# Optimization experiments

Measured on AMD Instinct MI355X. Metric: run time of the kernel, lower is better.

## Reference

```python
import jax, jax.numpy as jnp
import numpy as np

E = 2048
H = 16
D = E // H  # head_dim = 128


def setup_inputs() -> dict:
    key = jax.random.key(0)
    ks = jax.random.split(key, 8)
    s = 0.02
    x = jax.random.normal(ks[0], (2, 2048, E), dtype=jnp.float32)
    Wq = jax.random.normal(ks[1], (E, E), dtype=jnp.float32) * s
    Wk = jax.random.normal(ks[2], (E, E), dtype=jnp.float32) * s
    Wv = jax.random.normal(ks[3], (E, E), dtype=jnp.float32) * s
    W1 = jax.random.normal(ks[4], (2 * E, E), dtype=jnp.float32) * s
    b1 = jax.random.normal(ks[5], (2 * E,), dtype=jnp.float32) * s
    W2 = jax.random.normal(ks[6], (E, 2 * E), dtype=jnp.float32) * s
    b2 = jax.random.normal(ks[7], (E,), dtype=jnp.float32) * s
    return {"x": x, "Wq": Wq, "Wk": Wk, "Wv": Wv, "W1": W1, "b1": b1, "W2": W2, "b2": b2}


def reference(x, Wq, Wk, Wv, W1, b1, W2, b2):
    B, S, _ = x.shape
    # QKV projections (torch Linear: x @ W.T), reshape to (B,S,H,D)
    q = (x @ Wq.T).reshape(B, S, H, D)
    k = (x @ Wk.T).reshape(B, S, H, D)
    v = (x @ Wv.T).reshape(B, S, H, D)
    # scores: (B,H,S,S)
    score = jnp.einsum('bqhd,bkhd->bhqk', q, k)
    # causal mask added BEFORE scaling (as in original; -inf unaffected by scale)
    causal = jnp.tril(jnp.ones((S, S), dtype=bool))
    score = jnp.where(causal, score, -jnp.inf)
    score = score / jnp.sqrt(jnp.float32(D))
    attn = jax.nn.softmax(score, axis=-1)
    o = jnp.einsum('bhqk,bkhd->bqhd', attn, v).reshape(B, S, E)
    # FFN with hidden = 2*E, no residual connections in this block
    h = jax.nn.gelu(o @ W1.T + b1)
    return h @ W2.T + b2
```

## Files before the change

kernel.cpp:

```cpp
#include <hip/hip_runtime.h>
#include <cmath>


typedef _Float16 half8 __attribute__((ext_vector_type(8)));
typedef _Float16 half4v __attribute__((ext_vector_type(4)));
typedef float float4v __attribute__((ext_vector_type(4)));

__device__ inline void load_lds16(const _Float16* g, _Float16* l) {
  __builtin_amdgcn_global_load_lds(
      (const __attribute__((address_space(1))) void*)g,
      (__attribute__((address_space(3))) void*)l, 16, 0, 0);
}

__global__ void cvt_kernel(const float* __restrict__ s0, const float* __restrict__ s1,
                           const float* __restrict__ s2, const float* __restrict__ s3,
                           _Float16* d0, _Float16* d1, _Float16* d2, _Float16* d3,
                           int n0, int n1, int n2, int n3, float sc1) {
  const float* s;
  _Float16* d;
  int n;
  float sc = 1.0f;
  switch (blockIdx.y) {
    case 0: s = s0; d = d0; n = n0; break;
    case 1: s = s1; d = d1; n = n1; sc = sc1; break;
    case 2: s = s2; d = d2; n = n2; break;
    default: s = s3; d = d3; n = n3; break;
  }
  const int step = gridDim.x * 256 * 4;
  for (int i = (blockIdx.x * 256 + threadIdx.x) * 4; i < n; i += step) {
    float4v v = *(const float4v*)&s[i];
    half4v h;
#pragma unroll
    for (int e = 0; e < 4; e++) h[e] = (_Float16)(v[e] * sc);
    *(half4v*)&d[i] = h;
  }
}

__device__ inline void gemm_core(const _Float16* __restrict__ A,
                                 const _Float16* __restrict__ B, int K, int bm,
                                 int bn, _Float16* As, _Float16* Bs,
                                 float4v acc[4][4]) {
  const int tid = threadIdx.x;
  const int wave = tid >> 6, lane = tid & 63;
  const int l16 = lane & 15, quad = lane >> 4;
  const int wm = (wave & 1) * 64, wn = (wave >> 1) * 64;
  const int r0 = tid >> 2, c0 = (tid & 3) * 8;
  const int lds0 = (wave * 64) * 8;
  const int lds1 = (256 + wave * 64) * 8;

  for (int k0 = 0; k0 < K; k0 += 32) {
    load_lds16(&A[(size_t)(bm + r0) * K + k0 + c0], &As[lds0]);
    load_lds16(&A[(size_t)(bm + 64 + r0) * K + k0 + c0], &As[lds1]);
    load_lds16(&B[(size_t)(bn + r0) * K + k0 + c0], &Bs[lds0]);
    load_lds16(&B[(size_t)(bn + 64 + r0) * K + k0 + c0], &Bs[lds1]);
    __syncthreads();

    half8 af[4], bf[4];
#pragma unroll
    for (int i = 0; i < 4; i++)
      af[i] = *(const half8*)&As[(wm + i * 16 + l16) * 32 + quad * 8];
#pragma unroll
    for (int j = 0; j < 4; j++)
      bf[j] = *(const half8*)&Bs[(wn + j * 16 + l16) * 32 + quad * 8];

#pragma unroll
    for (int i = 0; i < 4; i++)
#pragma unroll
      for (int j = 0; j < 4; j++)
        acc[i][j] = __builtin_amdgcn_mfma_f32_16x16x32_f16(af[i], bf[j], acc[i][j], 0, 0, 0);
    __syncthreads();
  }
}

__global__ __launch_bounds__(256, 3) void gemm_qkv(
    const _Float16* __restrict__ xh, const _Float16* __restrict__ Wq,
    const _Float16* __restrict__ Wk, const _Float16* __restrict__ Wv,
    _Float16* __restrict__ Qh, _Float16* __restrict__ Kh,
    _Float16* __restrict__ Vt) {
  __shared__ __align__(16) _Float16 As[4096];
  __shared__ __align__(16) _Float16 Bs[4096];
  const int z = blockIdx.z;
  const _Float16* B = (z == 0) ? Wq : (z == 1 ? Wk : Wv);
  const int bm = blockIdx.y * 128, bn = blockIdx.x * 128;
  float4v acc[4][4] = {};
  gemm_core(xh, B, 2048, bm, bn, As, Bs, acc);

  const int tid = threadIdx.x;
  const int wave = tid >> 6, lane = tid & 63;
  const int l16 = lane & 15, quad = lane >> 4;
  const int wm = (wave & 1) * 64, wn = (wave >> 1) * 64;
  _Float16* outRM = z ? Kh : Qh;
#pragma unroll
  for (int j = 0; j < 4; j++) {
    const int col = bn + wn + j * 16 + l16;
#pragma unroll
    for (int i = 0; i < 4; i++) {
      const int rbase = bm + wm + i * 16 + quad * 4;
#pragma unroll
      for (int reg = 0; reg < 4; reg++) {
        const int m = rbase + reg;
        const _Float16 hv = (_Float16)acc[i][j][reg];
        if (z == 2)
          Vt[((size_t)(m >> 11) << 22) + ((size_t)col << 11) + (m & 2047)] = hv;
        else
          outRM[(size_t)m * 2048 + col] = hv;
      }
    }
  }
}

template <bool GELU>
__global__ __launch_bounds__(256, 3) void gemm_ffn(
    const _Float16* __restrict__ A, const _Float16* __restrict__ B,
    const float* __restrict__ bias, void* __restrict__ out, int M, int N,
    int K) {
  __shared__ __align__(16) _Float16 As[4096];
  __shared__ __align__(16) _Float16 Bs[4096];
  const int bm = blockIdx.y * 128, bn = blockIdx.x * 128;
  float4v acc[4][4] = {};
  gemm_core(A, B, K, bm, bn, As, Bs, acc);

  const int tid = threadIdx.x;
  const int wave = tid >> 6, lane = tid & 63;
  const int l16 = lane & 15, quad = lane >> 4;
  const int wm = (wave & 1) * 64, wn = (wave >> 1) * 64;
#pragma unroll
  for (int j = 0; j < 4; j++) {
    const int col = bn + wn + j * 16 + l16;
    const float bv = bias[col];
#pragma unroll
    for (int i = 0; i < 4; i++) {
      const int rbase = bm + wm + i * 16 + quad * 4;
#pragma unroll
      for (int reg = 0; reg < 4; reg++) {
        const int m = rbase + reg;
        float v = acc[i][j][reg] + bv;
        if (GELU) {
          const float x = v;
          const float inner = 0.7978845608028654f * (x + 0.044715f * x * x * x);
          v = 0.5f * x * (1.0f + tanhf(inner));
          ((_Float16*)out)[(size_t)m * N + col] = (_Float16)v;
        } else {
          ((float*)out)[(size_t)m * N + col] = v;
        }
      }
    }
  }
}

__global__ __launch_bounds__(256, 2) void attn_mfma(
    const _Float16* __restrict__ Qh, const _Float16* __restrict__ Kh,
    const _Float16* __restrict__ Vt, _Float16* __restrict__ Oh) {
  __shared__ __align__(16) _Float16 Ksh[64][136];
  __shared__ __align__(16) _Float16 Vsh[128][72];
  __shared__ __align__(16) _Float16 Psh[4][32][72];

  const int b = blockIdx.z;
  int qt = blockIdx.x;
  if (b) qt = gridDim.x - 1 - qt;
  const int h = blockIdx.y;
  const int tid = threadIdx.x;
  const int wave = tid >> 6, lane = tid & 63;
  const int l16 = lane & 15, quad = lane >> 4;
  const int q0 = qt * 128;
  const int wq0 = q0 + wave * 32;

  half8 qf[2][4];
#pragma unroll
  for (int rb = 0; rb < 2; rb++)
#pragma unroll
    for (int kc = 0; kc < 4; kc++)
      qf[rb][kc] = *(const half8*)(Qh +
          (size_t)(b * 2048 + wq0 + rb * 16 + l16) * 2048 + h * 128 +
          kc * 32 + quad * 8);

  half8 ones;
#pragma unroll
  for (int e = 0; e < 8; e++) ones[e] = (_Float16)1.0f;

  const int kkey = tid >> 2, kd = (tid & 3) * 32;
  const int vd = tid >> 1, vkey = (tid & 1) * 32;

  half8 kpre[4], vpre[4];
  {
    const _Float16* p = Kh + (size_t)(b * 2048 + kkey) * 2048 + h * 128 + kd;
#pragma unroll
    for (int i = 0; i < 4; i++) kpre[i] = *(const half8*)(p + i * 8);
    const _Float16* pv = Vt + ((size_t)b << 22) + (size_t)(h * 128 + vd) * 2048 + vkey;
#pragma unroll
    for (int i = 0; i < 4; i++) vpre[i] = *(const half8*)(pv + i * 8);
  }

  float4v o[2][9] = {};
  float4v mrow[2];
#pragma unroll
  for (int rb = 0; rb < 2; rb++)
#pragma unroll
    for (int e = 0; e < 4; e++) mrow[rb][e] = -INFINITY;

  const int nkb = qt * 2 + 2;
  for (int kb = 0; kb < nkb; kb++) {
    const int k0 = kb * 64;
    __syncthreads();
#pragma unroll
    for (int i = 0; i < 4; i++) *(half8*)&Ksh[kkey][kd + i * 8] = kpre[i];
#pragma unroll
    for (int i = 0; i < 4; i++) *(half8*)&Vsh[vd][vkey + i * 8] = vpre[i];
    __syncthreads();

    if (kb + 1 < nkb) {
      const int k1 = k0 + 64;
      const _Float16* p = Kh + (size_t)(b * 2048 + k1 + kkey) * 2048 + h * 128 + kd;
#pragma unroll
      for (int i = 0; i < 4; i++) kpre[i] = *(const half8*)(p + i * 8);
      const _Float16* pv = Vt + ((size_t)b << 22) + (size_t)(h * 128 + vd) * 2048 + k1 + vkey;
#pragma unroll
      for (int i = 0; i < 4; i++) vpre[i] = *(const half8*)(pv + i * 8);
    }

    if (k0 <= wq0 + 31) {
      float4v s[2][4] = {};
#pragma unroll
      for (int kc = 0; kc < 4; kc++) {
#pragma unroll
        for (int cb = 0; cb < 4; cb++) {
          half8 kf = *(const half8*)&Ksh[cb * 16 + l16][kc * 32 + quad * 8];
#pragma unroll
          for (int rb = 0; rb < 2; rb++)
            s[rb][cb] = __builtin_amdgcn_mfma_f32_16x16x32_f16(qf[rb][kc], kf, s[rb][cb], 0, 0, 0);
        }
      }
      if (k0 + 63 > wq0) {
#pragma unroll
        for (int cb = 0; cb < 4; cb++)
#pragma unroll
          for (int rb = 0; rb < 2; rb++)
#pragma unroll
            for (int reg = 0; reg < 4; reg++) {
              const int key = k0 + cb * 16 + l16;
              const int row = wq0 + rb * 16 + quad * 4 + reg;
              if (key > row) s[rb][cb][reg] = -INFINITY;
            }
      }
#pragma unroll
      for (int rb = 0; rb < 2; rb++) {
        float4v mt;
#pragma unroll
        for (int e = 0; e < 4; e++)
          mt[e] = fmaxf(fmaxf(s[rb][0][e], s[rb][1][e]),
                        fmaxf(s[rb][2][e], s[rb][3][e]));
#pragma unroll
        for (int msk = 1; msk <= 8; msk <<= 1)
#pragma unroll
          for (int e = 0; e < 4; e++) mt[e] = fmaxf(mt[e], __shfl_xor(mt[e], msk, 64));
        int need = 0;
#pragma unroll
        for (int e = 0; e < 4; e++) need |= (mt[e] > mrow[rb][e] + 8.0f) ? 1 : 0;
        if (__any(need)) {
          float4v al;
#pragma unroll
          for (int e = 0; e < 4; e++) {
            const float mn = fmaxf(mrow[rb][e], mt[e]);
            al[e] = exp2f(mrow[rb][e] - mn);
            mrow[rb][e] = mn;
          }
#pragma unroll
          for (int cd = 0; cd < 9; cd++)
#pragma unroll
            for (int e = 0; e < 4; e++) o[rb][cd][e] *= al[e];
        }
#pragma unroll
        for (int cb = 0; cb < 4; cb++) {
#pragma unroll
          for (int e = 0; e < 4; e++) s[rb][cb][e] = exp2f(s[rb][cb][e] - mrow[rb][e]);
#pragma unroll
          for (int e = 0; e < 4; e++)
            Psh[wave][rb * 16 + quad * 4 + e][cb * 16 + l16] = (_Float16)s[rb][cb][e];
        }
      }
      half8 pf[2][2];
#pragma unroll
      for (int rb = 0; rb < 2; rb++)
#pragma unroll
        for (int kc = 0; kc < 2; kc++)
          pf[rb][kc] = *(const half8*)&Psh[wave][rb * 16 + l16][kc * 32 + quad * 8];
#pragma unroll
      for (int cd = 0; cd < 8; cd++) {
#pragma unroll
        for (int kc = 0; kc < 2; kc++) {
          half8 vf = *(const half8*)&Vsh[cd * 16 + l16][kc * 32 + quad * 8];
#pragma unroll
          for (int rb = 0; rb < 2; rb++)
            o[rb][cd] = __builtin_amdgcn_mfma_f32_16x16x32_f16(pf[rb][kc], vf, o[rb][cd], 0, 0, 0);
        }
      }
#pragma unroll
      for (int kc = 0; kc < 2; kc++)
#pragma unroll
        for (int rb = 0; rb < 2; rb++)
          o[rb][8] = __builtin_amdgcn_mfma_f32_16x16x32_f16(pf[rb][kc], ones, o[rb][8], 0, 0, 0);
    }
  }

#pragma unroll
  for (int rb = 0; rb < 2; rb++) {
    float4v inv;
#pragma unroll
    for (int e = 0; e < 4; e++) inv[e] = 1.0f / o[rb][8][e];
#pragma unroll
    for (int cd = 0; cd < 8; cd++)
#pragma unroll
      for (int reg = 0; reg < 4; reg++)
        Oh[(size_t)(b * 2048 + wq0 + rb * 16 + quad * 4 + reg) * 2048 +
           h * 128 + cd * 16 + l16] = (_Float16)(o[rb][cd][reg] * inv[reg]);
  }
}

extern "C" void kernel_launch(void* const* d_in, const int* in_sizes, int n_in,
                              void* d_out, int out_size, void* d_ws,
                              size_t ws_size, hipStream_t stream) {
  const float* x = (const float*)d_in[0];
  const float* Wq = (const float*)d_in[1];
  const float* Wk = (const float*)d_in[2];
  const float* Wv = (const float*)d_in[3];
  const float* W1 = (const float*)d_in[4];
  const float* b1 = (const float*)d_in[5];
  const float* W2 = (const float*)d_in[6];
  const float* b2 = (const float*)d_in[7];
  float* out = (float*)d_out;

  const int ME = 8388608;
  const int EE = 4194304;

  _Float16* ws = (_Float16*)d_ws;
  _Float16* xh  = ws;
  _Float16* Wqh = xh + ME;
  _Float16* Wkh = Wqh + EE;
  _Float16* Wvh = Wkh + EE;
  _Float16* Qh  = Wvh + EE;
  _Float16* Kh  = Qh + ME;
  _Float16* Vt  = Kh + ME;
  _Float16* Oh  = xh;
  _Float16* W1h = Wqh;
  _Float16* W2h = Vt;
  _Float16* Hid = Qh;

  const float qscale = 1.4426950408889634f * 0.08838834764831845f;

  cvt_kernel<<<dim3(1024, 4), 256, 0, stream>>>(x, Wq, Wk, Wv, xh, Wqh, Wkh, Wvh,
                                                ME, EE, EE, EE, qscale);
  gemm_qkv<<<dim3(16, 32, 3), 256, 0, stream>>>(xh, Wqh, Wkh, Wvh, Qh, Kh, Vt);
  attn_mfma<<<dim3(16, 16, 2), 256, 0, stream>>>(Qh, Kh, Vt, Oh);
  cvt_kernel<<<dim3(1024, 2), 256, 0, stream>>>(W1, W2, nullptr, nullptr,
                                                W1h, W2h, nullptr, nullptr,
                                                ME, ME, 0, 0, 1.0f);
  gemm_ffn<true><<<dim3(32, 32), 256, 0, stream>>>(Oh, W1h, b1, Hid, 4096, 4096, 2048);
  gemm_ffn<false><<<dim3(16, 32), 256, 0, stream>>>(Hid, W2h, b2, out, 4096, 2048, 4096);
}
```

Before: 602.5 us.

## Replace GEMM core with 256x256 tiles, 8 waves and double-buffered LDS pipeline

Swaps the simple 128x128, 4-wave GEMM core for a 256x256 tile core run by 512 threads. It double-buffers 64-wide K slices in 128KB of LDS, interleaves async global-to-LDS loads with MFMA quarters under explicit barriers and waitcnts, and swizzles the LDS layout to avoid bank conflicts. The aim is more data reuse per tile and memory latency hidden behind MFMA work in all three projection/FFN GEMMs. The cost is fewer blocks (256 for the smaller GEMMs on 256 CUs) and high register and LDS pressure, and the hand-tuned barrier schedule is fragile to get right.

```diff
diff --git a/kernel.cpp b/kernel.cpp
--- a/kernel.cpp
+++ b/kernel.cpp
@@ -36,70 +36,147 @@
   }
 }
 
-__device__ inline void gemm_core(const _Float16* __restrict__ A,
-                                 const _Float16* __restrict__ B, int K, int bm,
-                                 int bn, _Float16* As, _Float16* Bs,
-                                 float4v acc[4][4]) {
+__device__ __forceinline__ void gemm8_core(
+    const _Float16* __restrict__ A, const _Float16* __restrict__ B, int K,
+    int bm, int bn, _Float16* lds, float4v acc[8][4]) {
   const int tid = threadIdx.x;
-  const int wave = tid >> 6, lane = tid & 63;
+  const int w = tid >> 6, lane = tid & 63;
   const int l16 = lane & 15, quad = lane >> 4;
-  const int wm = (wave & 1) * 64, wn = (wave >> 1) * 64;
-  const int r0 = tid >> 2, c0 = (tid & 3) * 8;
-  const int lds0 = (wave * 64) * 8;
-  const int lds1 = (256 + wave * 64) * 8;
-
-  for (int k0 = 0; k0 < K; k0 += 32) {
-    load_lds16(&A[(size_t)(bm + r0) * K + k0 + c0], &As[lds0]);
-    load_lds16(&A[(size_t)(bm + 64 + r0) * K + k0 + c0], &As[lds1]);
-    load_lds16(&B[(size_t)(bn + r0) * K + k0 + c0], &Bs[lds0]);
-    load_lds16(&B[(size_t)(bn + 64 + r0) * K + k0 + c0], &Bs[lds1]);
-    __syncthreads();
-
-    half8 af[4], bf[4];
-#pragma unroll
-    for (int i = 0; i < 4; i++)
-      af[i] = *(const half8*)&As[(wm + i * 16 + l16) * 32 + quad * 8];
-#pragma unroll
-    for (int j = 0; j < 4; j++)
-      bf[j] = *(const half8*)&Bs[(wn + j * 16 + l16) * 32 + quad * 8];
-
-#pragma unroll
-    for (int i = 0; i < 4; i++)
-#pragma unroll
-      for (int j = 0; j < 4; j++)
-        acc[i][j] = __builtin_amdgcn_mfma_f32_16x16x32_f16(af[i], bf[j], acc[i][j], 0, 0, 0);
-    __syncthreads();
-  }
-}
-
-__global__ __launch_bounds__(256, 3) void gemm_qkv(
+  const int srow = w * 16 + (lane >> 2);
+  const int clocal = ((lane & 3) * 8) ^ ((lane & 32) ? 16 : 0);
+  int rdh = (l16 << 5) + (quad << 3);
+  rdh ^= (l16 & 8) << 1;
+
+  const _Float16* pA0 = A + (size_t)(bm + srow) * K + clocal;
+  const _Float16* pA1 = A + (size_t)(bm + 128 + srow) * K + clocal;
+  const _Float16* pB0 = B + (size_t)(bn + srow) * K + clocal;
+  const _Float16* pB1 = B + (size_t)(bn + 128 + srow) * K + clocal;
+
+  _Float16* const dA0 = lds + w * 1024;
+  _Float16* const dA1 = lds + 8192 + w * 1024;
+  _Float16* const dB0 = lds + 16384 + w * 1024;
+  _Float16* const dB1 = lds + 24576 + w * 1024;
+
+  const int aH = w >> 2, bH = (w >> 1) & 1, bRB = (w & 1) * 4;
+  const _Float16* const rA0 = lds + aH * 8192;
+  const _Float16* const rB0 = lds + 16384 + bH * 8192;
+  const _Float16* const rA1 = rA0 + 32768;
+  const _Float16* const rB1 = rB0 + 32768;
+
+  const int NT = K >> 6;
+
+#define STG(p, d, kt)                     \
+  do {                                    \
+    const _Float16* _s = (p) + (kt) * 64; \
+    load_lds16(_s, (d));                  \
+    load_lds16(_s + 32, (d) + 512);       \
+  } while (0)
+#define BARRIER() asm volatile("s_barrier" ::: "memory")
+#define WAIT_LGKM()                                  \
+  asm volatile("s_waitcnt lgkmcnt(0)" ::: "memory"); \
+  __builtin_amdgcn_sched_barrier(0);
+#define RD_A(base, RB0)                                                       \
+  _Pragma("unroll") for (int rb = 0; rb < 4; rb++)                            \
+  _Pragma("unroll") for (int ks = 0; ks < 2; ks++)                            \
+      af[rb][ks] = *(const half8*)&(base)[((((RB0) + rb) * 2 + ks) << 9) + rdh];
+#define RD_B(base, J0)                                                        \
+  _Pragma("unroll") for (int j = 0; j < 2; j++)                               \
+  _Pragma("unroll") for (int ks = 0; ks < 2; ks++)                            \
+      bf[(J0) + j][ks] =                                                      \
+          *(const half8*)&(base)[(((bRB + (J0) + j) * 2 + ks) << 9) + rdh];
+#define MFMA_Q(RB0, J0)                                                       \
+  __builtin_amdgcn_s_setprio(1);                                              \
+  _Pragma("unroll") for (int rb = 0; rb < 4; rb++)                            \
+  _Pragma("unroll") for (int j = 0; j < 2; j++)                               \
+  _Pragma("unroll") for (int ks = 0; ks < 2; ks++)                            \
+      acc[(RB0) + rb][(J0) + j] = __builtin_amdgcn_mfma_f32_16x16x32_f16(     \
+          af[rb][ks], bf[(J0) + j][ks], acc[(RB0) + rb][(J0) + j], 0, 0, 0);  \
+  __builtin_amdgcn_s_setprio(0);                                              \
+  BARRIER();
+
+  STG(pB0, dB0, 0); STG(pB1, dB1, 0); STG(pA0, dA0, 0); STG(pA1, dA1, 0);
+  STG(pB0, dB0 + 32768, 1); STG(pB1, dB1 + 32768, 1);
+  asm volatile("s_waitcnt vmcnt(4)" ::: "memory");
+  BARRIER();
+
+  half8 af[4][2], bf[4][2];
+
+  for (int t = 0; t < NT; t += 2) {
+    const bool last = (t + 2 >= NT);
+    RD_A(rA0, 0) RD_B(rB0, 0)
+    STG(pA0, dA0 + 32768, t + 1);
+    BARRIER(); WAIT_LGKM()
+    MFMA_Q(0, 0)
+    RD_B(rB0, 2)
+    STG(pA1, dA1 + 32768, t + 1);
+    BARRIER(); WAIT_LGKM()
+    MFMA_Q(0, 2)
+    RD_A(rA0, 4)
+    if (!last) STG(pB0, dB0, t + 2);
+    BARRIER(); WAIT_LGKM()
+    MFMA_Q(4, 0)
+    if (!last) {
+      STG(pA0, dA0, t + 2);
+      asm volatile("s_waitcnt vmcnt(4)" ::: "memory");
+    } else {
+      asm volatile("s_waitcnt vmcnt(0)" ::: "memory");
+    }
+    BARRIER();
+    MFMA_Q(4, 2)
+    RD_A(rA1, 0) RD_B(rB1, 0)
+    if (!last) STG(pA1, dA1, t + 2);
+    BARRIER(); WAIT_LGKM()
+    MFMA_Q(0, 0)
+    RD_B(rB1, 2)
+    if (!last) STG(pB1, dB1, t + 2);
+    BARRIER(); WAIT_LGKM()
+    MFMA_Q(0, 2)
+    RD_A(rA1, 4)
+    if (!last) STG(pB0, dB0 + 32768, t + 3);
+    BARRIER(); WAIT_LGKM()
+    MFMA_Q(4, 0)
+    if (!last) {
+      STG(pB1, dB1 + 32768, t + 3);
+      asm volatile("s_waitcnt vmcnt(4)" ::: "memory");
+    }
+    BARRIER();
+    MFMA_Q(4, 2)
+  }
+#undef STG
+#undef BARRIER
+#undef WAIT_LGKM
+#undef RD_A
+#undef RD_B
+#undef MFMA_Q
+}
+
+__global__ __launch_bounds__(512, 2) void gemm_qkv(
     const _Float16* __restrict__ xh, const _Float16* __restrict__ Wq,
     const _Float16* __restrict__ Wk, const _Float16* __restrict__ Wv,
     _Float16* __restrict__ Qh, _Float16* __restrict__ Kh,
     _Float16* __restrict__ Vt) {
-  __shared__ __align__(16) _Float16 As[4096];
-  __shared__ __align__(16) _Float16 Bs[4096];
+  __shared__ __align__(16) _Float16 lds[65536];
   const int z = blockIdx.z;
   const _Float16* B = (z == 0) ? Wq : (z == 1 ? Wk : Wv);
-  const int bm = blockIdx.y * 128, bn = blockIdx.x * 128;
-  float4v acc[4][4] = {};
-  gemm_core(xh, B, 2048, bm, bn, As, Bs, acc);
+  const int bm = blockIdx.y * 256, bn = blockIdx.x * 256;
+  float4v acc[8][4] = {};
+  gemm8_core(xh, B, 2048, bm, bn, lds, acc);
 
   const int tid = threadIdx.x;
-  const int wave = tid >> 6, lane = tid & 63;
+  const int w = tid >> 6, lane = tid & 63;
   const int l16 = lane & 15, quad = lane >> 4;
-  const int wm = (wave & 1) * 64, wn = (wave >> 1) * 64;
+  const int wm = (w >> 2) * 128, wn = (w & 3) * 64;
   _Float16* outRM = z ? Kh : Qh;
 #pragma unroll
   for (int j = 0; j < 4; j++) {
     const int col = bn + wn + j * 16 + l16;
 #pragma unroll
-    for (int i = 0; i < 4; i++) {
-      const int rbase = bm + wm + i * 16 + quad * 4;
+    for (int rb = 0; rb < 8; rb++) {
+      const int rbase = bm + wm + rb * 16 + quad * 4;
 #pragma unroll
       for (int reg = 0; reg < 4; reg++) {
         const int m = rbase + reg;
-        const _Float16 hv = (_Float16)acc[i][j][reg];
+        const _Float16 hv = (_Float16)acc[rb][j][reg];
         if (z == 2)
           Vt[((size_t)(m >> 11) << 22) + ((size_t)col << 11) + (m & 2047)] = hv;
         else
@@ -110,31 +187,29 @@
 }
 
 template <bool GELU>
-__global__ __launch_bounds__(256, 3) void gemm_ffn(
+__global__ __launch_bounds__(512, 2) void gemm_ffn(
     const _Float16* __restrict__ A, const _Float16* __restrict__ B,
-    const float* __restrict__ bias, void* __restrict__ out, int M, int N,
-    int K) {
-  __shared__ __align__(16) _Float16 As[4096];
-  __shared__ __align__(16) _Float16 Bs[4096];
-  const int bm = blockIdx.y * 128, bn = blockIdx.x * 128;
-  float4v acc[4][4] = {};
-  gemm_core(A, B, K, bm, bn, As, Bs, acc);
+    const float* __restrict__ bias, void* __restrict__ out, int N, int K) {
+  __shared__ __align__(16) _Float16 lds[65536];
+  const int bm = blockIdx.y * 256, bn = blockIdx.x * 256;
+  float4v acc[8][4] = {};
+  gemm8_core(A, B, K, bm, bn, lds, acc);
 
   const int tid = threadIdx.x;
-  const int wave = tid >> 6, lane = tid & 63;
+  const int w = tid >> 6, lane = tid & 63;
   const int l16 = lane & 15, quad = lane >> 4;
-  const int wm = (wave & 1) * 64, wn = (wave >> 1) * 64;
+  const int wm = (w >> 2) * 128, wn = (w & 3) * 64;
 #pragma unroll
   for (int j = 0; j < 4; j++) {
     const int col = bn + wn + j * 16 + l16;
     const float bv = bias[col];
 #pragma unroll
-    for (int i = 0; i < 4; i++) {
-      const int rbase = bm + wm + i * 16 + quad * 4;
+    for (int rb = 0; rb < 8; rb++) {
+      const int rbase = bm + wm + rb * 16 + quad * 4;
 #pragma unroll
       for (int reg = 0; reg < 4; reg++) {
         const int m = rbase + reg;
-        float v = acc[i][j][reg] + bv;
+        float v = acc[rb][j][reg] + bv;
         if (GELU) {
           const float x = v;
           const float inner = 0.7978845608028654f * (x + 0.044715f * x * x * x);
@@ -349,11 +424,11 @@
 
   cvt_kernel<<<dim3(1024, 4), 256, 0, stream>>>(x, Wq, Wk, Wv, xh, Wqh, Wkh, Wvh,
                                                 ME, EE, EE, EE, qscale);
-  gemm_qkv<<<dim3(16, 32, 3), 256, 0, stream>>>(xh, Wqh, Wkh, Wvh, Qh, Kh, Vt);
+  gemm_qkv<<<dim3(8, 16, 3), 512, 0, stream>>>(xh, Wqh, Wkh, Wvh, Qh, Kh, Vt);
   attn_mfma<<<dim3(16, 16, 2), 256, 0, stream>>>(Qh, Kh, Vt, Oh);
   cvt_kernel<<<dim3(1024, 2), 256, 0, stream>>>(W1, W2, nullptr, nullptr,
                                                 W1h, W2h, nullptr, nullptr,
                                                 ME, ME, 0, 0, 1.0f);
-  gemm_ffn<true><<<dim3(32, 32), 256, 0, stream>>>(Oh, W1h, b1, Hid, 4096, 4096, 2048);
-  gemm_ffn<false><<<dim3(16, 32), 256, 0, stream>>>(Hid, W2h, b2, out, 4096, 2048, 4096);
-}
+  gemm_ffn<true><<<dim3(16, 16), 512, 0, stream>>>(Oh, W1h, b1, Hid, 4096, 2048);
+  gemm_ffn<false><<<dim3(8, 16), 512, 0, stream>>>(Hid, W2h, b2, out, 2048, 4096);
+}
```

New measurement: 601.6 us. No clear change (-0.1%).
